# Kernel tuning notes

Measured on AMD Instinct MI355X. Metric: run time of the kernel, lower is better.

Reference implementation:

```python
import jax, jax.numpy as jnp
import numpy as np

T = 262144  # time steps (~700 years daily)
HID = 32    # M100 hidden width


def setup_inputs() -> dict:
    key = jax.random.key(0)
    ks = jax.random.split(key, 10)
    # forward arg: inputs [T, 5] = [s_snow, s_water, precp, tmean, time]
    s_snow = jax.random.uniform(ks[0], (T,), jnp.float32) * 10.0
    s_water = jax.random.uniform(ks[1], (T,), jnp.float32) * 100.0
    precp = jax.random.uniform(ks[2], (T,), jnp.float32) * 10.0   # mm/day, >=0
    tmean = jax.random.normal(ks[3], (T,), jnp.float32) * 10.0    # deg C
    time = jnp.arange(T, dtype=jnp.float32)                       # integer day grid
    inputs = jnp.stack([s_snow, s_water, precp, tmean, time], axis=-1)
    # forward arg: day-length forcing (separate interpolator in original)
    lday = jax.random.uniform(ks[4], (T,), jnp.float32) * 0.5 + 0.2
    # M100 MLP params: 4 -> 32 -> 32 -> 5, tanh hidden
    scale = 0.2
    W1 = jax.random.normal(ks[5], (4, HID), jnp.float32) * scale
    b1 = jnp.zeros((HID,), jnp.float32)
    W2 = jax.random.normal(ks[6], (HID, HID), jnp.float32) * scale
    b2 = jnp.zeros((HID,), jnp.float32)
    W3 = jax.random.normal(ks[7], (HID, 5), jnp.float32) * scale
    b3 = jnp.zeros((5,), jnp.float32)
    return {"inputs": inputs, "lday": lday, "W1": W1, "b1": b1,
            "W2": W2, "b2": b2, "W3": W3, "b3": b3}


def reference(inputs, lday, W1, b1, W2, b2, W3, b3):
    precp = inputs[:, 2]
    tmean = inputs[:, 3]
    time = inputs[:, 4]
    n = precp.shape[0]

    def step_fn(x):
        return (jnp.tanh(5.0 * x) + 1.0) * 0.5

    def mlp(x):  # works on [4] or [N,4]
        h = jnp.tanh(x @ W1 + b1)
        h = jnp.tanh(h @ W2 + b2)
        return h @ W3 + b3

    def interp(f, t):  # periodic linear interpolation on the unit day grid
        i0 = jnp.floor(t)
        frac = t - i0
        i = jnp.mod(i0.astype(jnp.int32), n)
        ip = jnp.mod(i + 1, n)
        return f[i] * (1.0 - frac) + f[ip] * frac

    def rhs(t, y):  # hybrid_model_mlp: MLP-parameterized ExpHydro fluxes
        s0, s1 = y[0], y[1]
        p = interp(precp, t)
        tm = interp(tmean, t)
        ld = interp(lday, t)
        o = mlp(jnp.stack([s0, s1, p, tm]))
        p_snow = jax.nn.relu(jnp.sinh(o[0]) * step_fn(-tm))
        p_rain = jax.nn.relu(jnp.sinh(o[1]))
        m = jax.nn.relu(step_fn(s0) * jnp.sinh(o[2]))
        et = step_fn(s1) * jnp.exp(o[3]) * ld
        q = step_fn(s1) * jnp.exp(o[4])
        return jnp.stack([p_snow - m, p_rain + m - et - q])

    y0 = jnp.stack([inputs[0, 0], inputs[0, 1]])  # [2]
    t0s = time[:-1]
    dts = time[1:] - time[:-1]

    def scan_step(y, tdt):  # classic RK4 step between saved time points
        t, dt = tdt
        k1 = rhs(t, y)
        k2 = rhs(t + 0.5 * dt, y + 0.5 * dt * k1)
        k3 = rhs(t + 0.5 * dt, y + 0.5 * dt * k2)
        k4 = rhs(t + dt, y + dt * k3)
        yn = y + (dt / 6.0) * (k1 + 2.0 * k2 + 2.0 * k3 + k4)
        return yn, yn

    _, ys = jax.lax.scan(scan_step, y0, (t0s, dts))
    ys = jnp.concatenate([y0[None, :], ys], axis=0)  # [T, 2]

    s_snow_nn = jnp.maximum(ys[:, 0], 0.0)
    s_water_nn = jnp.maximum(ys[:, 1], 0.0)
    inputs_nn = jnp.stack([s_snow_nn, s_water_nn, precp, tmean], axis=-1)  # [T, 4]
    out = mlp(inputs_nn)  # [T, 5]
    return out[:, -1]      # q head
```

## Files before the change

### kernel.cpp

```cpp
#include <hip/hip_runtime.h>
#include <math.h>

#define T_TOTAL 262144
#define HID 32
#define WIN 3072
#define NSWEEP 6
#define CH 1024
#define FD_EPS0 4.0
#define FD_EPS1 8.0
#define LOG2E 1.4426950408889634f
#define TANH2C 2.8853900817779268f
#define NEG10LOG2E (-14.426950408889634f)
#define POS10LOG2E (14.426950408889634f)

#define PIN(x) asm volatile("" : "+v"(x))

typedef _Float16 f16x8 __attribute__((ext_vector_type(8)));
typedef float f32x4 __attribute__((ext_vector_type(4)));

__device__ __forceinline__ float fexp2(float x) { return __builtin_amdgcn_exp2f(x); }
__device__ __forceinline__ float frcp(float x)  { return __builtin_amdgcn_rcpf(x); }
__device__ __forceinline__ float fast_sig10(float x) {
    return frcp(1.0f + fexp2(x * NEG10LOG2E));
}
__device__ __forceinline__ float fast_tanh_clamp(float x) {
    float xc = __builtin_amdgcn_fmed3f(x, -9.0f, 9.0f);
    float u  = fexp2(xc * TANH2C);
    return fmaf(-2.0f, frcp(u + 1.0f), 1.0f);
}
__device__ __forceinline__ float fast_tanh_nc(float x) {
    float u = fexp2(x * TANH2C);
    return fmaf(-2.0f, frcp(u + 1.0f), 1.0f);
}

template <int CTRL>
__device__ __forceinline__ float dpp_add(float v) {
    int t = __builtin_amdgcn_update_dpp(0, __float_as_int(v), CTRL, 0xF, 0xF, true);
    return v + __int_as_float(t);
}
__device__ __forceinline__ float allsum16(float x) {
    x = dpp_add<0xB1>(x);
    x = dpp_add<0x4E>(x);
    x = dpp_add<0x141>(x);
    x = dpp_add<0x140>(x);
    return x;
}
__device__ __forceinline__ int dpp_xor1_i(int v) {
    return __builtin_amdgcn_update_dpp(0, v, 0xB1, 0xF, 0xF, true);
}
__device__ __forceinline__ float rl(float x, int lane) {
    return __int_as_float(__builtin_amdgcn_readlane(__float_as_int(x), lane));
}
__device__ __forceinline__ float bpf(int addr, float x) {
    return __int_as_float(__builtin_amdgcn_ds_bpermute(addr, __float_as_int(x)));
}

__global__ void init_kernel(const float* __restrict__ inputs, float2* icg) {
    int w = blockIdx.x * blockDim.x + threadIdx.x;
    if (w < WIN) icg[w] = make_float2(inputs[0], inputs[1]);
}

__global__ __launch_bounds__(64, 1) void sweep_kernel(
    const float* __restrict__ inputs,
    const float* __restrict__ lday,
    const float* __restrict__ W1, const float* __restrict__ b1,
    const float* __restrict__ W2, const float* __restrict__ b2,
    const float* __restrict__ W3, const float* __restrict__ b3,
    float* __restrict__ traj,
    const float2* __restrict__ icg,
    double2* __restrict__ E)
{
    const int lane = threadIdx.x;
    const int col  = lane & 15;
    const int quad = lane >> 4;
    const int j32  = lane & 31;
    const int half = lane >> 5;
    const bool odd = (lane & 1) != 0;

    const int wnd  = blockIdx.x;
    const int S    = wnd * 85 + ((wnd < 1024) ? wnd : 1024);
    const int LEN  = (wnd < 1024) ? 86 : 85;
    const int endStep = (S + LEN < T_TOTAL - 1) ? (S + LEN) : (T_TOTAL - 1);

    float w1c0 = W1[0 * HID + j32] * TANH2C, w1c1 = W1[1 * HID + j32] * TANH2C;
    float w1c2 = W1[2 * HID + j32] * TANH2C, w1c3 = W1[3 * HID + j32] * TANH2C;
    float b1j = b1[j32] * TANH2C;
    PIN(w1c0); PIN(w1c1); PIN(w1c2); PIN(w1c3); PIN(b1j);

    f16x8 Bhi0, Blo0, Bhi1, Blo1;
#pragma unroll
    for (int jj = 0; jj < 8; ++jj) {
        float w0 = W2[(quad * 8 + jj) * HID + col] * TANH2C;
        float w1v = W2[(quad * 8 + jj) * HID + col + 16] * TANH2C;
        _Float16 h0 = (_Float16)w0, h1v = (_Float16)w1v;
        Bhi0[jj] = h0;  Blo0[jj] = (_Float16)(w0 - (float)h0);
        Bhi1[jj] = h1v; Blo1[jj] = (_Float16)(w1v - (float)h1v);
    }
    PIN(Bhi0); PIN(Blo0); PIN(Bhi1); PIN(Blo1);

    float b2a2 = b2[col] * TANH2C, b2b2 = b2[col + 16] * TANH2C;
    f32x4 cb0 = {b2a2, b2a2, b2a2, b2a2};
    f32x4 cb1 = {b2b2, b2b2, b2b2, b2b2};
    PIN(cb0); PIN(cb1);

    float wca[5], wcb[5];
#pragma unroll
    for (int c = 0; c < 5; ++c) {
        wca[c] = W3[col * 5 + c] * LOG2E;
        wcb[c] = W3[(col + 16) * 5 + c] * LOG2E;
        PIN(wca[c]); PIN(wcb[c]);
    }

    float m0 = (col == 0) ? 1.f : 0.f;
    float m1 = (col == 1) ? 1.f : 0.f;
    float m2 = (col == 2) ? 1.f : 0.f;
    float m3 = (col == 3) ? 1.f : 0.f;
    float m4 = (col == 4) ? 1.f : 0.f;
    float m5 = (col == 5) ? 1.f : 0.f;
    float m6 = (col == 6) ? 1.f : 0.f;
    float m7 = (col == 7) ? 1.f : 0.f;
    float m8 = (col == 8) ? 1.f : 0.f;
    float sig1m = (col >= 5 && col <= 8) ? 1.f : 0.f;
    float zb = b3[(col < 5) ? col : 0];
    float zconst = (col < 5) ? zb * LOG2E : 0.f;
    PIN(m0); PIN(m1); PIN(m2); PIN(m3); PIN(m4); PIN(m5); PIN(m6); PIN(m7); PIN(m8);
    PIN(sig1m); PIN(zconst);

    int psel = (lane & 1) ? 0x01000504 : 0x05040100;
    int l3 = lane & 3;
    int roff = (l3 == 1) ? 128 : (l3 == 2) ? 4 : (l3 == 3) ? 132 : 0;
    int bbase = 32 * quad + roff;
    int bp0 = bbase, bp1 = bbase + 8, bp2 = bbase + 16, bp3 = bbase + 24;
    PIN(psel); PIN(bp0); PIN(bp1); PIN(bp2); PIN(bp3);

    int qb = 64 * quad;
    int a_sh0 = qb + 0,  a_sh1 = qb + 4,  a_sh2 = qb + 8;
    int a_e3  = qb + 12, a_e4  = qb + 16, a_sg0 = qb + 20, a_sg1 = qb + 24;
    PIN(a_sh0); PIN(a_sh1); PIN(a_sh2); PIN(a_e3); PIN(a_e4); PIN(a_sg0); PIN(a_sg1);

    float2 ic = icg[wnd];
    double y0 = (double)ic.x + ((quad == 1) ? FD_EPS0 : 0.0);
    double y1 = (double)ic.y + ((quad >= 2) ? FD_EPS1 : 0.0);
    float2* traj2 = (float2*)traj;
    if (lane == 0 && wnd == 0)
        traj2[0] = make_float2(ic.x, ic.y);

    auto rhs = [&](float s0q, float s1q, float base, float stm, float ld, float zoffk,
                   float& d0, float& d1, float& rout) {
        float s0A = rl(s0q, 0),  s1A = rl(s1q, 0);
        float s0B = rl(s0q, 16), s1B = rl(s1q, 16);
        float s0C = rl(s0q, 32), s1C = rl(s1q, 32);
        float s0p = half ? s0B : s0A;
        float s1p = half ? s1B : s1A;
        float prep = fmaf(s1p, w1c1, fmaf(s0p, w1c0, base));
        float prec = fmaf(s1C, w1c1, fmaf(s0C, w1c0, base));
        float up_ = fexp2(prep);
        float uc_ = fexp2(prec);
        float h1p = fmaf(-2.0f, frcp(up_ + 1.0f), 1.0f);
        float h1c = fmaf(-2.0f, frcp(uc_ + 1.0f), 1.0f);
        union { _Float16 h; unsigned short u; } cvp, cvc;
        cvp.h = (_Float16)h1p; cvc.h = (_Float16)h1c;
        int ownp = (int)cvp.u, ownc = (int)cvc.u;
        int nbp = dpp_xor1_i(ownp), nbc = dpp_xor1_i(ownc);
        int pkp = __builtin_amdgcn_perm(nbp, ownp, psel);
        int pkc = __builtin_amdgcn_perm(nbc, ownc, psel);
        int pk  = odd ? pkc : pkp;
        int g0i = __builtin_amdgcn_ds_bpermute(bp0, pk);
        int g1i = __builtin_amdgcn_ds_bpermute(bp1, pk);
        int g2i = __builtin_amdgcn_ds_bpermute(bp2, pk);
        int g3i = __builtin_amdgcn_ds_bpermute(bp3, pk);
        union { int i[4]; f16x8 h; } au;
        au.i[0] = g0i; au.i[1] = g1i; au.i[2] = g2i; au.i[3] = g3i;
        f16x8 A = au.h;
        f32x4 zz = {0.f, 0.f, 0.f, 0.f};
        f32x4 chi0 = __builtin_amdgcn_mfma_f32_16x16x32_f16(A, Bhi0, cb0, 0, 0, 0);
        f32x4 clo0 = __builtin_amdgcn_mfma_f32_16x16x32_f16(A, Blo0, zz, 0, 0, 0);
        f32x4 chi1 = __builtin_amdgcn_mfma_f32_16x16x32_f16(A, Bhi1, cb1, 0, 0, 0);
        f32x4 clo1 = __builtin_amdgcn_mfma_f32_16x16x32_f16(A, Blo1, zz, 0, 0, 0);
        float tA0 = chi0[0] + clo0[0], tB0 = chi0[1] + clo0[1], tC0 = chi0[2] + clo0[2];
        float tA1 = chi1[0] + clo1[0], tB1 = chi1[1] + clo1[1], tC1 = chi1[2] + clo1[2];
        float t0 = (quad == 1) ? tB0 : (quad >= 2) ? tC0 : tA0;
        float t1 = (quad == 1) ? tB1 : (quad >= 2) ? tC1 : tA1;
        float ua = fexp2(t0);
        float ub = fexp2(t1);
        float g0 = fmaf(-2.0f, frcp(ua + 1.0f), 1.0f);
        float g1 = fmaf(-2.0f, frcp(ub + 1.0f), 1.0f);
        float r0 = fmaf(g0, wca[0], g1 * wcb[0]);
        float r1 = fmaf(g0, wca[1], g1 * wcb[1]);
        float r2 = fmaf(g0, wca[2], g1 * wcb[2]);
        float r3 = fmaf(g0, wca[3], g1 * wcb[3]);
        float r4 = fmaf(g0, wca[4], g1 * wcb[4]);
        float s0r = allsum16(r0);
        float s1r = allsum16(r1);
        float s2r = allsum16(r2);
        float s3r = allsum16(r3);
        float s4r = allsum16(r4);
        float zs0 = s0q * NEG10LOG2E;
        float zs1 = s1q * NEG10LOG2E;
        float zoff = fmaf(zs0, m5, fmaf(zs1, m6, zoffk));
        float zarg = fmaf(s0r, m0, fmaf(s1r, m1, fmaf(s2r, m2,
                     fmaf(s3r, m3, fmaf(s4r, m4, zoff)))));
        float u = fexp2(zarg);
        float r = frcp(u + sig1m);
        float w = fmaf(0.5f, u, -0.5f * r);
        float sh0 = bpf(a_sh0, w), sh1 = bpf(a_sh1, w), sh2 = bpf(a_sh2, w);
        float e3  = bpf(a_e3, u),  e4  = bpf(a_e4, u);
        float sg0 = bpf(a_sg0, r), sg1 = bpf(a_sg1, r);
        float p_snow = fmaxf(sh0 * stm, 0.f);
        float p_rain = fmaxf(sh1, 0.f);
        float melt   = fmaxf(sg0 * sh2, 0.f);
        float etq    = sg1 * fmaf(e3, ld, e4);
        d0 = p_snow - melt;
        d1 = (p_rain + melt) - etq;
        rout = r;
    };

    float pA = inputs[S * 5 + 2],       tmA = inputs[S * 5 + 3],       ldA = lday[S];
    float pB = inputs[(S + 1) * 5 + 2], tmB = inputs[(S + 1) * 5 + 3], ldB = lday[S + 1];
    float pC = inputs[(S + 2) * 5 + 2], tmC = inputs[(S + 2) * 5 + 3], ldC = lday[S + 2];
    float stmA = fast_sig10(-tmA);
    float stmB = fast_sig10(-tmB);
    float stmm = fast_sig10(-0.5f * (tmA + tmB));
    float baseA = fmaf(pA, w1c2, fmaf(tmA, w1c3, b1j));
    float baseB = fmaf(pB, w1c2, fmaf(tmB, w1c3, b1j));

    for (int n = S; n < endStep; ++n) {
        const float ldm = 0.5f * (ldA + ldB);
        const float pm  = 0.5f * (pA + pB);
        const float tmm = 0.5f * (tmA + tmB);
        const float basem = fmaf(pm, w1c2, fmaf(tmm, w1c3, b1j));
        const float ztm_m = (0.5f * (tmB + tmC)) * POS10LOG2E;
        const float ztm_b = tmC * POS10LOG2E;
        const float zoffk = fmaf(ztm_m, m7, fmaf(ztm_b, m8, zconst));

        const float fy0 = (float)y0, fy1 = (float)y1;
        float k10, k11, k20, k21, k30, k31, k40, k41, rd;
        rhs(fy0,                  fy1,                  baseA, stmA, ldA, zoffk, k10, k11, rd);
        rhs(fmaf(0.5f, k10, fy0), fmaf(0.5f, k11, fy1), basem, stmm, ldm, zoffk, k20, k21, rd);
        rhs(fmaf(0.5f, k20, fy0), fmaf(0.5f, k21, fy1), basem, stmm, ldm, zoffk, k30, k31, rd);
        rhs(fy0 + k30,            fy1 + k31,            baseB, stmB, ldB, zoffk, k40, k41, rd);
        const float stmm_n = rl(rd, 7);
        const float stmB_n = rl(rd, 8);

        const float s0sum = (k10 + 2.0f * k20) + (2.0f * k30 + k40);
        const float s1sum = (k11 + 2.0f * k21) + (2.0f * k31 + k41);
        y0 += (1.0 / 6.0) * (double)s0sum;
        y1 += (1.0 / 6.0) * (double)s1sum;

        if (lane == 0)
            traj2[n + 1] = make_float2((float)y0, (float)y1);

        stmA = stmB; stmB = stmB_n; stmm = stmm_n;
        baseA = baseB;
        baseB = fmaf(pC, w1c2, fmaf(tmC, w1c3, b1j));
        pA = pB; tmA = tmB; ldA = ldB;
        pB = pC; tmB = tmC; ldB = ldC;
        const int np3 = (n + 3 < T_TOTAL) ? (n + 3) : (T_TOTAL - 1);
        pC = inputs[np3 * 5 + 2]; tmC = inputs[np3 * 5 + 3]; ldC = lday[np3];
    }

    if (lane == 0)  E[wnd]           = make_double2(y0, y1);
    if (lane == 16) E[WIN + wnd]     = make_double2(y0, y1);
    if (lane == 32) E[2 * WIN + wnd] = make_double2(y0, y1);
}

__global__ __launch_bounds__(128) void correct_kernel(
    const float* __restrict__ inputs,
    const double2* __restrict__ E,
    float2* __restrict__ icg) {
    __shared__ float sJ00[2][CH], sJ10[2][CH], sJ11[2][CH];
    __shared__ float sE0x[2][CH], sE0y[2][CH];
    __shared__ float sGx[2][CH],  sGy[2][CH];
    const int tid = threadIdx.x;

    auto stage_one = [&](int buf, int i, int w) {
        double2 e0 = E[w];
        double2 e1 = E[WIN + w];
        double2 e2 = E[2 * WIN + w];
        float2 g   = icg[w];
        float J00 = (float)((e1.x - e0.x) * (1.0 / FD_EPS0));
        float J10 = (float)((e1.y - e0.y) * (1.0 / FD_EPS0));
        float J11 = (float)((e2.y - e0.y) * (1.0 / FD_EPS1));
        sJ00[buf][i] = fminf(fmaxf(J00, -0.15f), 1.15f);
        sJ10[buf][i] = fminf(fmaxf(J10, -0.30f), 1.80f);
        sJ11[buf][i] = fminf(fmaxf(J11,  0.00f), 1.10f);
        sE0x[buf][i] = (float)e0.x; sE0y[buf][i] = (float)e0.y;
        sGx[buf][i]  = g.x;         sGy[buf][i]  = g.y;
    };

    for (int i = tid; i < CH; i += 128) stage_one(0, i, i);
    __syncthreads();

    float y0c = inputs[0];
    float y1c = inputs[1];
    for (int c = 0; c < 3; ++c) {
        const int buf = c & 1;
        if (tid == 0) {
            const int wbase = c * CH;
#pragma unroll 8
            for (int i = 0; i < CH; ++i) {
                float d0 = y0c - sGx[buf][i];
                float d1 = y1c - sGy[buf][i];
                d0 = fminf(fmaxf(d0, -50.0f), 50.0f);
                d1 = fminf(fmaxf(d1, -400.0f), 400.0f);
                icg[wbase + i] = make_float2(y0c, y1c);
                y0c = fmaf(sJ00[buf][i], d0, sE0x[buf][i]);
                y1c = fmaf(sJ10[buf][i], d0, fmaf(sJ11[buf][i], d1, sE0y[buf][i]));
                y0c = fminf(fmaxf(y0c, -5.0f), 1000.0f);
                y1c = fminf(fmaxf(y1c, -5.0f), 5000.0f);
            }
        } else if (tid >= 64 && c + 1 < 3) {
            for (int i = tid - 64; i < CH; i += 64)
                stage_one((c + 1) & 1, i, (c + 1) * CH + i);
        }
        __syncthreads();
    }
}

__global__ __launch_bounds__(256) void out_kernel(
    const float* __restrict__ inputs,
    const float* __restrict__ traj,
    const float* __restrict__ W1, const float* __restrict__ b1,
    const float* __restrict__ W2, const float* __restrict__ b2,
    const float* __restrict__ W3, const float* __restrict__ b3,
    float* __restrict__ out)
{
    __shared__ float sW1[4 * HID];
    __shared__ float sb1[HID];
    __shared__ float sW2T[HID * HID];
    __shared__ float sb2[HID];
    __shared__ float sw3[HID];
    for (int i = threadIdx.x; i < 4 * HID; i += 256) sW1[i] = W1[i];
    for (int i = threadIdx.x; i < HID; i += 256) {
        sb1[i] = b1[i]; sb2[i] = b2[i]; sw3[i] = W3[i * 5 + 4];
    }
    for (int idx = threadIdx.x; idx < HID * HID; idx += 256) {
        int jj = idx >> 5, ii = idx & 31;
        sW2T[idx] = W2[ii * HID + jj];
    }
    __syncthreads();

    int t = blockIdx.x * 256 + threadIdx.x;
    if (t >= T_TOTAL) return;

    float2 st = ((const float2*)traj)[t];
    float s0 = fmaxf(st.x, 0.0f);
    float s1 = fmaxf(st.y, 0.0f);
    float p  = inputs[t * 5 + 2];
    float tm = inputs[t * 5 + 3];

    float h1[HID];
#pragma unroll
    for (int jj = 0; jj < HID; ++jj) {
        float pre = fmaf(s0, sW1[jj], fmaf(s1, sW1[HID + jj],
                    fmaf(p, sW1[2 * HID + jj],
                    fmaf(tm, sW1[3 * HID + jj], sb1[jj]))));
        h1[jj] = fast_tanh_clamp(pre);
    }
    float o = b3[4];
#pragma unroll 4
    for (int jj = 0; jj < HID; ++jj) {
        float a0 = sb2[jj], a1 = 0.f, a2 = 0.f, a3 = 0.f;
#pragma unroll
        for (int ii = 0; ii < HID; ii += 4) {
            a0 = fmaf(h1[ii + 0], sW2T[jj * HID + ii + 0], a0);
            a1 = fmaf(h1[ii + 1], sW2T[jj * HID + ii + 1], a1);
            a2 = fmaf(h1[ii + 2], sW2T[jj * HID + ii + 2], a2);
            a3 = fmaf(h1[ii + 3], sW2T[jj * HID + ii + 3], a3);
        }
        o = fmaf(fast_tanh_nc((a0 + a1) + (a2 + a3)), sw3[jj], o);
    }
    out[t] = o;
}

extern "C" void kernel_launch(void* const* d_in, const int* in_sizes, int n_in,
                              void* d_out, int out_size, void* d_ws, size_t ws_size,
                              hipStream_t stream) {
    (void)in_sizes; (void)n_in; (void)out_size; (void)ws_size;
    const float* inputs = (const float*)d_in[0];
    const float* lday   = (const float*)d_in[1];
    const float* W1     = (const float*)d_in[2];
    const float* b1     = (const float*)d_in[3];
    const float* W2     = (const float*)d_in[4];
    const float* b2     = (const float*)d_in[5];
    const float* W3     = (const float*)d_in[6];
    const float* b3     = (const float*)d_in[7];
    float* out  = (float*)d_out;
    float* traj = (float*)d_ws;

    char* scr = (char*)d_out;
    double2* E  = (double2*)scr;
    float2* icg = (float2*)(scr + 196608);

    hipLaunchKernelGGL(init_kernel, dim3((WIN + 255) / 256), dim3(256), 0, stream,
                       inputs, icg);
    for (int k = 0; k < NSWEEP - 1; ++k) {
        hipLaunchKernelGGL(sweep_kernel, dim3(WIN), dim3(64), 0, stream,
                           inputs, lday, W1, b1, W2, b2, W3, b3, traj, icg, E);
        hipLaunchKernelGGL(correct_kernel, dim3(1), dim3(128), 0, stream,
                           inputs, E, icg);
    }
    hipLaunchKernelGGL(sweep_kernel, dim3(WIN), dim3(64), 0, stream,
                       inputs, lday, W1, b1, W2, b2, W3, b3, traj, icg, E);
    hipLaunchKernelGGL(out_kernel, dim3((T_TOTAL + 255) / 256), dim3(256), 0, stream,
                       inputs, traj, W1, b1, W2, b2, W3, b3, out);
}
```

Before: 2.209 ms.

## Use the fourth MFMA row for a Richardson-extrapolated Jacobian and drop one sweep

The fourth quad of the wavefront, previously a duplicate, now integrates an extra perturbed trajectory with a smaller s_water offset. The correction kernel combines the two perturbations into a Richardson-extrapolated J11 estimate. With a more accurate Newton/parareal Jacobian, the number of sweep iterations is cut from six to five, removing one full sweep and correct launch pair. This adds a little per-step work (one more exp/rcp and shuffle) and a larger scratch area, and relies on the better Jacobian keeping convergence within tolerance after fewer sweeps.

Result: faster. 2.034 ms (-7.9%).

```diff
diff --git a/kernel.cpp b/kernel.cpp
--- a/kernel.cpp
+++ b/kernel.cpp
@@ -4,10 +4,11 @@
 #define T_TOTAL 262144
 #define HID 32
 #define WIN 3072
-#define NSWEEP 6
+#define NSWEEP 5
 #define CH 1024
 #define FD_EPS0 4.0
 #define FD_EPS1 8.0
+#define FD_EPS1B 4.0
 #define LOG2E 1.4426950408889634f
 #define TANH2C 2.8853900817779268f
 #define NEG10LOG2E (-14.426950408889634f)
@@ -140,7 +141,8 @@
 
     float2 ic = icg[wnd];
     double y0 = (double)ic.x + ((quad == 1) ? FD_EPS0 : 0.0);
-    double y1 = (double)ic.y + ((quad >= 2) ? FD_EPS1 : 0.0);
+    double y1 = (double)ic.y +
+                ((quad == 2) ? FD_EPS1 : (quad == 3) ? FD_EPS1B : 0.0);
     float2* traj2 = (float2*)traj;
     if (lane == 0 && wnd == 0)
         traj2[0] = make_float2(ic.x, ic.y);
@@ -150,21 +152,26 @@
         float s0A = rl(s0q, 0),  s1A = rl(s1q, 0);
         float s0B = rl(s0q, 16), s1B = rl(s1q, 16);
         float s0C = rl(s0q, 32), s1C = rl(s1q, 32);
+        float s0D = rl(s0q, 48), s1D = rl(s1q, 48);
         float s0p = half ? s0B : s0A;
         float s1p = half ? s1B : s1A;
         float prep = fmaf(s1p, w1c1, fmaf(s0p, w1c0, base));
         float prec = fmaf(s1C, w1c1, fmaf(s0C, w1c0, base));
+        float pred = fmaf(s1D, w1c1, fmaf(s0D, w1c0, base));
         float up_ = fexp2(prep);
         float uc_ = fexp2(prec);
+        float ud_ = fexp2(pred);
         float h1p = fmaf(-2.0f, frcp(up_ + 1.0f), 1.0f);
         float h1c = fmaf(-2.0f, frcp(uc_ + 1.0f), 1.0f);
-        union { _Float16 h; unsigned short u; } cvp, cvc;
-        cvp.h = (_Float16)h1p; cvc.h = (_Float16)h1c;
-        int ownp = (int)cvp.u, ownc = (int)cvc.u;
-        int nbp = dpp_xor1_i(ownp), nbc = dpp_xor1_i(ownc);
+        float h1d = fmaf(-2.0f, frcp(ud_ + 1.0f), 1.0f);
+        union { _Float16 h; unsigned short u; } cvp, cvc, cvd;
+        cvp.h = (_Float16)h1p; cvc.h = (_Float16)h1c; cvd.h = (_Float16)h1d;
+        int ownp = (int)cvp.u, ownc = (int)cvc.u, ownd = (int)cvd.u;
+        int nbp = dpp_xor1_i(ownp), nbc = dpp_xor1_i(ownc), nbd = dpp_xor1_i(ownd);
         int pkp = __builtin_amdgcn_perm(nbp, ownp, psel);
         int pkc = __builtin_amdgcn_perm(nbc, ownc, psel);
-        int pk  = odd ? pkc : pkp;
+        int pkd = __builtin_amdgcn_perm(nbd, ownd, psel);
+        int pk  = odd ? (half ? pkd : pkc) : pkp;
         int g0i = __builtin_amdgcn_ds_bpermute(bp0, pk);
         int g1i = __builtin_amdgcn_ds_bpermute(bp1, pk);
         int g2i = __builtin_amdgcn_ds_bpermute(bp2, pk);
@@ -177,10 +184,12 @@
         f32x4 clo0 = __builtin_amdgcn_mfma_f32_16x16x32_f16(A, Blo0, zz, 0, 0, 0);
         f32x4 chi1 = __builtin_amdgcn_mfma_f32_16x16x32_f16(A, Bhi1, cb1, 0, 0, 0);
         f32x4 clo1 = __builtin_amdgcn_mfma_f32_16x16x32_f16(A, Blo1, zz, 0, 0, 0);
-        float tA0 = chi0[0] + clo0[0], tB0 = chi0[1] + clo0[1], tC0 = chi0[2] + clo0[2];
-        float tA1 = chi1[0] + clo1[0], tB1 = chi1[1] + clo1[1], tC1 = chi1[2] + clo1[2];
-        float t0 = (quad == 1) ? tB0 : (quad >= 2) ? tC0 : tA0;
-        float t1 = (quad == 1) ? tB1 : (quad >= 2) ? tC1 : tA1;
+        float tA0 = chi0[0] + clo0[0], tB0 = chi0[1] + clo0[1];
+        float tC0 = chi0[2] + clo0[2], tD0 = chi0[3] + clo0[3];
+        float tA1 = chi1[0] + clo1[0], tB1 = chi1[1] + clo1[1];
+        float tC1 = chi1[2] + clo1[2], tD1 = chi1[3] + clo1[3];
+        float t0 = (quad == 0) ? tA0 : (quad == 1) ? tB0 : (quad == 2) ? tC0 : tD0;
+        float t1 = (quad == 0) ? tA1 : (quad == 1) ? tB1 : (quad == 2) ? tC1 : tD1;
         float ua = fexp2(t0);
         float ub = fexp2(t1);
         float g0 = fmaf(-2.0f, frcp(ua + 1.0f), 1.0f);
@@ -262,6 +271,7 @@
     if (lane == 0)  E[wnd]           = make_double2(y0, y1);
     if (lane == 16) E[WIN + wnd]     = make_double2(y0, y1);
     if (lane == 32) E[2 * WIN + wnd] = make_double2(y0, y1);
+    if (lane == 48) E[3 * WIN + wnd] = make_double2(y0, y1);
 }
 
 __global__ __launch_bounds__(128) void correct_kernel(
@@ -277,10 +287,12 @@
         double2 e0 = E[w];
         double2 e1 = E[WIN + w];
         double2 e2 = E[2 * WIN + w];
+        double2 e3 = E[3 * WIN + w];
         float2 g   = icg[w];
         float J00 = (float)((e1.x - e0.x) * (1.0 / FD_EPS0));
         float J10 = (float)((e1.y - e0.y) * (1.0 / FD_EPS0));
-        float J11 = (float)((e2.y - e0.y) * (1.0 / FD_EPS1));
+        float J11 = (float)((e3.y - e0.y) * (2.0 / FD_EPS1B)
+                          - (e2.y - e0.y) * (1.0 / FD_EPS1));
         sJ00[buf][i] = fminf(fmaxf(J00, -0.15f), 1.15f);
         sJ10[buf][i] = fminf(fmaxf(J10, -0.30f), 1.80f);
         sJ11[buf][i] = fminf(fmaxf(J11,  0.00f), 1.10f);
@@ -390,7 +402,7 @@
 
     char* scr = (char*)d_out;
     double2* E  = (double2*)scr;
-    float2* icg = (float2*)(scr + 196608);
+    float2* icg = (float2*)(scr + 262144);
 
     hipLaunchKernelGGL(init_kernel, dim3((WIN + 255) / 256), dim3(256), 0, stream,
                        inputs, icg);
```
